# Optimization experiments

Hardware: AMD Instinct MI355X
Metric: run time of the kernel (lower is better)

## Reference

```python
import jax, jax.numpy as jnp
import numpy as np
from jax.scipy.special import logsumexp

D, V, B, N = 256, 10000, 16, 22
CF, CR, CA = 400, 120, 48   # num_func_cats, num_res_cats, num_arg_cats
NEG = -1e9


def setup_inputs() -> dict:
    key = jax.random.key(0)
    ks = jax.random.split(key, 12)
    s = 0.1
    return {
        "fake_emb": jnp.eye(CR, dtype=jnp.float32),  # nn.Parameter(torch.eye(num_res_cats))
        "nt_emb": jax.random.normal(ks[0], (CF, D), jnp.float32),
        "rule_W": jax.random.normal(ks[1], (2 * CA, CR), jnp.float32) * s,
        "rule_b": jnp.zeros((2 * CA,), jnp.float32),
        "root_w": jax.random.normal(ks[2], (CF,), jnp.float32) * s,  # root_mlp weight (input dim 1)
        "root_b": jnp.zeros((CF,), jnp.float32),
        "root_mask": jnp.zeros((CF,), jnp.float32),  # can_be_root mask (0 = allowed)
        "split_W1": jax.random.normal(ks[3], (D, D), jnp.float32) * s,
        "split_b1": jnp.zeros((D,), jnp.float32),
        "res_W": jax.random.normal(ks[4], (2, 2, D, D), jnp.float32) * s,  # 2 ResidualLayers x 2 Linears
        "res_b": jnp.zeros((2, 2, D), jnp.float32),
        "split_Wo": jax.random.normal(ks[5], (D, 2), jnp.float32) * s,
        "split_bo": jnp.zeros((2,), jnp.float32),
        "emit_W": jax.random.normal(ks[6], (D, V), jnp.float32) * s,  # word emission head
        "emit_b": jnp.zeros((V,), jnp.float32),
        "words": jax.random.randint(ks[7], (B, N), 0, V),
        "lfunc_ixs": jax.random.randint(ks[8], (CR, CA), 0, CF),
        "rfunc_ixs": jax.random.randint(ks[9], (CR, CA), 0, CF),
    }


def reference(fake_emb, nt_emb, rule_W, rule_b, root_w, root_b, root_mask,
              split_W1, split_b1, res_W, res_b, split_Wo, split_bo,
              emit_W, emit_b, words, lfunc_ixs, rfunc_ixs):
    # ---- grammar scores (set_grammar branch) ----
    # root_mlp(eye(1)).squeeze() == root_w + root_b
    root_scores = jax.nn.log_softmax(root_mask + root_w + root_b)          # [CF]
    rule_scores = jax.nn.log_softmax(fake_emb @ rule_W.T + rule_b, axis=1)  # [CR, 2*CA]

    # split_mlp: Linear -> ResidualLayer x2 -> Linear(D,2)
    h = nt_emb @ split_W1 + split_b1
    for i in range(2):  # fixed small layer loop
        t = jax.nn.relu(h @ res_W[i, 0] + res_b[i, 0])
        h = jax.nn.relu(t @ res_W[i, 1] + res_b[i, 1]) + h
    split_scores = jax.nn.log_softmax(h @ split_Wo + split_bo, axis=1)      # [CF, 2]

    gL = rule_scores[:, :CA] + split_scores[:CR, 0:1]  # full_G_larg [CR, CA]
    gR = rule_scores[:, CA:] + split_scores[:CR, 0:1]  # full_G_rarg [CR, CA]

    # ---- emission model: log p(word | category) gathered per token ----
    word_lp = jax.nn.log_softmax(nt_emb @ emit_W + emit_b, axis=-1)  # [CF, V]
    emit = word_lp[:, words]                                         # [CF, B, N]
    term = (split_scores[:, 1][:, None, None] + emit).transpose(2, 1, 0)  # [N, B, CF]

    # ---- CKY inside pass: beta[i, j, b, cat] over spans ----
    beta = jnp.full((N, N, B, CF), NEG, jnp.float32)
    d = jnp.arange(N)
    beta = beta.at[d, d].set(term)

    for w in range(2, N + 1):  # recurrence over span widths (static)
        S = N - w + 1
        st = np.arange(S)[:, None]          # span starts [S,1]
        kk = np.arange(1, w)[None, :]       # split points [1,w-1]
        left = beta[st, st + kk - 1]                                   # [S,w-1,B,CF]
        right = beta[st + kk, np.broadcast_to(st + w - 1, (S, w - 1))]  # [S,w-1,B,CF]
        # res -> arg(left) + rfunc(right)
        sL = gL + left[..., :CA][..., None, :] + right[..., rfunc_ixs]  # [S,w-1,B,CR,CA]
        # res -> lfunc(left) + arg(right)
        sR = gR + left[..., lfunc_ixs] + right[..., :CA][..., None, :]
        new = jnp.logaddexp(logsumexp(sL, axis=(1, 4)),
                            logsumexp(sR, axis=(1, 4)))                 # [S,B,CR]
        full = jnp.full((S, B, CF), NEG, jnp.float32).at[..., :CR].set(new)
        beta = beta.at[st[:, 0], st[:, 0] + w - 1].set(full)

    ll = logsumexp(root_scores + beta[0, N - 1], axis=-1)  # [B]
    return -ll  # logprob_list * -1
```

## Files before the change

kernel.cpp:

```cpp
#include <hip/hip_runtime.h>
#include <math.h>

#define D 256
#define V 10000
#define BB 16
#define NN 22
#define CF 400
#define CR 120
#define CA 48
#define CRP 121
#define PADF 20

__global__ void k_root(const float* __restrict__ root_w, const float* __restrict__ root_b,
                       const float* __restrict__ root_mask, float* __restrict__ root_scores) {
  __shared__ float red[512];
  int t = threadIdx.x;
  float x = (t < CF) ? (root_mask[t] + root_w[t] + root_b[t]) : -INFINITY;
  red[t] = x; __syncthreads();
  for (int off = 256; off; off >>= 1) { if (t < off) red[t] = fmaxf(red[t], red[t + off]); __syncthreads(); }
  float m = red[0]; __syncthreads();
  red[t] = (t < CF) ? __expf(x - m) : 0.f; __syncthreads();
  for (int off = 256; off; off >>= 1) { if (t < off) red[t] += red[t + off]; __syncthreads(); }
  float z = m + __logf(red[0]);
  if (t < CF) root_scores[t] = x - z;
}

__global__ __launch_bounds__(512) void k_mlp(const float* __restrict__ nt_emb, const float* __restrict__ W1,
                      const float* __restrict__ b1, const float* __restrict__ resW,
                      const float* __restrict__ resb, const float* __restrict__ Wo,
                      const float* __restrict__ bo, float* __restrict__ split_scores) {
  __shared__ float xs[2][D], hs[2][D], ts[2][D], prt[2][2][D];
  __shared__ float redg[2][4][2];
  int t = threadIdx.x; int c = t & 255; int h = t >> 8;
  int f0 = blockIdx.x * 2;
  xs[h][c] = nt_emb[(size_t)(f0 + h) * D + c];
  __syncthreads();
  int d0 = h * 128;
  float a0 = 0.f, a1 = 0.f;
#pragma unroll 8
  for (int dd = 0; dd < 128; dd++) {
    float wv = W1[(size_t)(d0 + dd) * D + c];
    a0 += xs[0][d0 + dd] * wv; a1 += xs[1][d0 + dd] * wv;
  }
  prt[0][h][c] = a0; prt[1][h][c] = a1;
  __syncthreads();
  if (h == 0) {
    float bv = b1[c];
    hs[0][c] = prt[0][0][c] + prt[0][1][c] + bv;
    hs[1][c] = prt[1][0][c] + prt[1][1][c] + bv;
  }
  __syncthreads();
  for (int il = 0; il < 2; il++) {
    const float* W = resW + (size_t)(il * 2) * D * D;
    a0 = 0.f; a1 = 0.f;
#pragma unroll 8
    for (int dd = 0; dd < 128; dd++) {
      float wv = W[(size_t)(d0 + dd) * D + c];
      a0 += hs[0][d0 + dd] * wv; a1 += hs[1][d0 + dd] * wv;
    }
    prt[0][h][c] = a0; prt[1][h][c] = a1;
    __syncthreads();
    if (h == 0) {
      float bv = resb[(il * 2) * D + c];
      ts[0][c] = fmaxf(prt[0][0][c] + prt[0][1][c] + bv, 0.f);
      ts[1][c] = fmaxf(prt[1][0][c] + prt[1][1][c] + bv, 0.f);
    }
    __syncthreads();
    const float* W2 = resW + (size_t)(il * 2 + 1) * D * D;
    a0 = 0.f; a1 = 0.f;
#pragma unroll 8
    for (int dd = 0; dd < 128; dd++) {
      float wv = W2[(size_t)(d0 + dd) * D + c];
      a0 += ts[0][d0 + dd] * wv; a1 += ts[1][d0 + dd] * wv;
    }
    prt[0][h][c] = a0; prt[1][h][c] = a1;
    __syncthreads();
    if (h == 0) {
      float bv = resb[(il * 2 + 1) * D + c];
      hs[0][c] = fmaxf(prt[0][0][c] + prt[0][1][c] + bv, 0.f) + hs[0][c];
      hs[1][c] = fmaxf(prt[1][0][c] + prt[1][1][c] + bv, 0.f) + hs[1][c];
    }
    __syncthreads();
  }
  float y0 = hs[h][c] * Wo[c * 2 + 0], y1 = hs[h][c] * Wo[c * 2 + 1];
  for (int off = 32; off; off >>= 1) { y0 += __shfl_down(y0, off, 64); y1 += __shfl_down(y1, off, 64); }
  int wq = (t >> 6) & 3;
  if ((t & 63) == 0) { redg[h][wq][0] = y0; redg[h][wq][1] = y1; }
  __syncthreads();
  if (c == 0) {
    float s0 = redg[h][0][0] + redg[h][1][0] + redg[h][2][0] + redg[h][3][0] + bo[0];
    float s1 = redg[h][0][1] + redg[h][1][1] + redg[h][2][1] + redg[h][3][1] + bo[1];
    float m = fmaxf(s0, s1);
    float z = m + __logf(__expf(s0 - m) + __expf(s1 - m));
    split_scores[(f0 + h) * 2 + 0] = s0 - z;
    split_scores[(f0 + h) * 2 + 1] = s1 - z;
  }
}

__global__ void k_glgr(const float* __restrict__ rule_W, const float* __restrict__ rule_b,
                       const float* __restrict__ split_scores,
                       const int* __restrict__ lf, const int* __restrict__ rf,
                       float4* __restrict__ rules) {
  __shared__ float red[128];
  __shared__ float shv[96];
  int r = blockIdx.x;
  int t = threadIdx.x;
  float x = (t < 96) ? (rule_W[t * CR + r] + rule_b[t]) : -INFINITY;
  red[t] = x; __syncthreads();
  for (int off = 64; off; off >>= 1) { if (t < off) red[t] = fmaxf(red[t], red[t + off]); __syncthreads(); }
  float m = red[0]; __syncthreads();
  red[t] = (t < 96) ? __expf(x - m) : 0.f; __syncthreads();
  for (int off = 64; off; off >>= 1) { if (t < off) red[t] += red[t + off]; __syncthreads(); }
  float z = m + __logf(red[0]);
  float s0 = split_scores[r * 2 + 0];
  if (t < 96) shv[t] = __expf((x - z) + s0);
  __syncthreads();
  if (t < CA) {
    float4 pk;
    pk.x = shv[t];
    pk.y = shv[CA + t];
    pk.z = __int_as_float(rf[r * CA + t]);
    pk.w = __int_as_float(lf[r * CA + t]);
    rules[r * CA + t] = pk;
  }
}

#define RT 8
__global__ __launch_bounds__(128) void k_emit_partial(const float* __restrict__ nt_emb,
                               const float* __restrict__ emit_W,
                               const float* __restrict__ emit_b, float* __restrict__ partial) {
  __shared__ float xs[RT][D];
  __shared__ float ldsw[RT][2];
  int t = threadIdx.x;
  int f0 = blockIdx.x * RT;
  int v0 = blockIdx.y * 512 + t * 4;
  for (int idx = t; idx < RT * D; idx += 128) {
    int ri = idx >> 8, d = idx & 255;
    xs[ri][d] = nt_emb[(size_t)(f0 + ri) * D + d];
  }
  __syncthreads();
  float psum[RT];
  for (int ri = 0; ri < RT; ri++) psum[ri] = 0.f;
  if (v0 < V) {
    float acc[RT][4];
#pragma unroll
    for (int ri = 0; ri < RT; ri++)
      for (int j = 0; j < 4; j++) acc[ri][j] = 0.f;
    for (int d4 = 0; d4 < D / 4; d4++) {
      float4 w0 = *(const float4*)(emit_W + (size_t)(4 * d4 + 0) * V + v0);
      float4 w1 = *(const float4*)(emit_W + (size_t)(4 * d4 + 1) * V + v0);
      float4 w2 = *(const float4*)(emit_W + (size_t)(4 * d4 + 2) * V + v0);
      float4 w3 = *(const float4*)(emit_W + (size_t)(4 * d4 + 3) * V + v0);
#pragma unroll
      for (int ri = 0; ri < RT; ri++) {
        float4 xv = *(const float4*)(&xs[ri][4 * d4]);
        acc[ri][0] += xv.x * w0.x + xv.y * w1.x + xv.z * w2.x + xv.w * w3.x;
        acc[ri][1] += xv.x * w0.y + xv.y * w1.y + xv.z * w2.y + xv.w * w3.y;
        acc[ri][2] += xv.x * w0.z + xv.y * w1.z + xv.z * w2.z + xv.w * w3.z;
        acc[ri][3] += xv.x * w0.w + xv.y * w1.w + xv.z * w2.w + xv.w * w3.w;
      }
    }
    float4 eb = *(const float4*)(emit_b + v0);
#pragma unroll
    for (int ri = 0; ri < RT; ri++)
      psum[ri] = __expf(acc[ri][0] + eb.x) + __expf(acc[ri][1] + eb.y) +
                 __expf(acc[ri][2] + eb.z) + __expf(acc[ri][3] + eb.w);
  }
  int lane = t & 63, wid = t >> 6;
  for (int ri = 0; ri < RT; ri++) {
    float v = psum[ri];
    for (int off = 32; off; off >>= 1) v += __shfl_down(v, off, 64);
    if (lane == 0) ldsw[ri][wid] = v;
  }
  __syncthreads();
  if (t < RT) partial[(f0 + t) * 32 + blockIdx.y] = ldsw[t][0] + ldsw[t][1];
}

__global__ void k_logz(const float* __restrict__ partial, float* __restrict__ logZ) {
  int t = blockIdx.x * blockDim.x + threadIdx.x;
  if (t < CF) {
    float s = 0.f;
    for (int ct = 0; ct < 20; ct++) s += partial[t * 32 + ct];
    logZ[t] = __logf(s);
  }
}

__global__ __launch_bounds__(512) void k_term(const float* __restrict__ nt_emb,
                       const float* __restrict__ emit_W,
                       const float* __restrict__ emit_b, const int* __restrict__ words,
                       const float* __restrict__ split_scores, const float* __restrict__ logZ,
                       float* __restrict__ ET, float* __restrict__ bmax) {
  __shared__ float vals[CF];
  __shared__ float redw[8];
  __shared__ float mfin;
  int blk = blockIdx.x;
  int b = blk / NN, n = blk % NN;
  int t = threadIdx.x;
  int lane = t & 63, wid = t >> 6;
  int wd = words[b * NN + n];
  float wc0 = emit_W[(size_t)(4 * lane + 0) * V + wd];
  float wc1 = emit_W[(size_t)(4 * lane + 1) * V + wd];
  float wc2 = emit_W[(size_t)(4 * lane + 2) * V + wd];
  float wc3 = emit_W[(size_t)(4 * lane + 3) * V + wd];
  float eb = emit_b[wd];
  float vmax = -INFINITY;
  int fbase = wid * 50;
  for (int k = 0; k < 50; k += 2) {
    int f0 = fbase + k, f1 = f0 + 1;
    float4 xa = *(const float4*)(nt_emb + (size_t)f0 * D + 4 * lane);
    float4 xb = *(const float4*)(nt_emb + (size_t)f1 * D + 4 * lane);
    float va = xa.x * wc0 + xa.y * wc1 + xa.z * wc2 + xa.w * wc3;
    float vb = xb.x * wc0 + xb.y * wc1 + xb.z * wc2 + xb.w * wc3;
    for (int off = 32; off; off >>= 1) {
      va += __shfl_down(va, off, 64);
      vb += __shfl_down(vb, off, 64);
    }
    if (lane == 0) {
      float fa = split_scores[f0 * 2 + 1] + (va + eb) - logZ[f0];
      float fb = split_scores[f1 * 2 + 1] + (vb + eb) - logZ[f1];
      vals[f0] = fa; vals[f1] = fb;
      vmax = fmaxf(vmax, fmaxf(fa, fb));
    }
  }
  if (lane == 0) redw[wid] = vmax;
  __syncthreads();
  if (t == 0) {
    float m = redw[0];
    for (int i2 = 1; i2 < 8; i2++) m = fmaxf(m, redw[i2]);
    mfin = m;
    bmax[(n * NN + n) * BB + b] = m;
  }
  __syncthreads();
  float m = mfin;
  for (int f = t; f < CF; f += 512) ET[((size_t)n * CF + f) * BB + b] = __expf(vals[f] - m);
}

__global__ __launch_bounds__(512) void k_cky_part(const float4* __restrict__ rules,
                      const float* __restrict__ ET, const float* __restrict__ EB,
                      const float* __restrict__ bmax, float* __restrict__ partial,
                      int w, int rsplit) {
  __shared__ float SL[CF * PADF];
  __shared__ float SR[CF * PADF];
  __shared__ float sMbuf[21 * BB];
  __shared__ float cks[BB];
  __shared__ float4 sred[512];
  int t = threadIdx.x;
  int blk = blockIdx.x;
  int rb = blk % rsplit; int rem = blk / rsplit;
  int wm1 = w - 1;
  int k = rem % wm1; int s = rem / wm1;
  int i = s, j = s + w - 1;
  bool ld = (k == 0), rd = (k == wm1 - 1);
  if (t < BB * wm1) {
    int k2 = t >> 4, b2 = t & 15;
    sMbuf[t] = bmax[(i * NN + (i + k2)) * BB + b2] + bmax[((i + k2 + 1) * NN + j) * BB + b2];
  }
  __syncthreads();
  if (t < BB) {
    float M = sMbuf[t];
    for (int k2 = 1; k2 < wm1; k2++) M = fmaxf(M, sMbuf[k2 * BB + t]);
    cks[t] = __expf(sMbuf[k * BB + t] - M);
  }
  const float* srcL = ld ? (ET + (size_t)i * CF * BB) : (EB + (size_t)(i * NN + (i + k)) * CRP * BB);
  const float* srcR = rd ? (ET + (size_t)j * CF * BB) : (EB + (size_t)((i + k + 1) * NN + j) * CRP * BB);
  int rowsL = ld ? CF : CRP, rowsR = rd ? CF : CRP;
  for (int idx = t; idx < rowsL * 4; idx += 512) {
    int f = idx >> 2, q = idx & 3;
    *(float4*)&SL[f * PADF + q * 4] = *(const float4*)&srcL[f * BB + q * 4];
  }
  for (int idx = t; idx < rowsR * 4; idx += 512) {
    int f = idx >> 2, q = idx & 3;
    *(float4*)&SR[f * PADF + q * 4] = *(const float4*)&srcR[f * BB + q * 4];
  }
  __syncthreads();
  int nr = CR / rsplit;
  int asplit = 128 / nr;
  int bq = t & 3, rr = t >> 2;
  float4 acc = {0.f, 0.f, 0.f, 0.f};
  bool act = (rr < nr * asplit);
  int rloc = rr % nr, asub = rr / nr;
  int r = rb * nr + rloc;
  if (act) {
    int na = CA / asplit;
    const float4* rp = rules + (size_t)r * CA + asub * na;
    int boff = bq * 4;
    int aB = asub * na;
#pragma unroll 4
    for (int a0 = 0; a0 < na; a0++) {
      float4 rule = rp[a0];
      int a = aB + a0;
      int fL = __float_as_int(rule.z);
      int fR = __float_as_int(rule.w);
      int fLc = rd ? fL : min(fL, 120);
      int fRc = ld ? fR : min(fR, 120);
      float4 La = *(const float4*)&SL[a * PADF + boff];
      float4 Ra = *(const float4*)&SR[a * PADF + boff];
      float4 Rg = *(const float4*)&SR[fLc * PADF + boff];
      float4 Lg = *(const float4*)&SL[fRc * PADF + boff];
      acc.x += rule.x * (La.x * Rg.x) + rule.y * (Lg.x * Ra.x);
      acc.y += rule.x * (La.y * Rg.y) + rule.y * (Lg.y * Ra.y);
      acc.z += rule.x * (La.z * Rg.z) + rule.y * (Lg.z * Ra.z);
      acc.w += rule.x * (La.w * Rg.w) + rule.y * (Lg.w * Ra.w);
    }
  }
  if (asplit > 1) {
    sred[t] = acc;
    __syncthreads();
    if (act && asub == 0) {
      for (int s2 = 1; s2 < asplit; s2++) {
        float4 o = sred[t + s2 * nr * 4];
        acc.x += o.x; acc.y += o.y; acc.z += o.z; acc.w += o.w;
      }
    }
  }
  if (act && asub == 0) {
    float4 c4 = *(const float4*)&cks[bq * 4];
    acc.x *= c4.x; acc.y *= c4.y; acc.z *= c4.z; acc.w *= c4.w;
    *(float4*)&partial[(((size_t)s * 21 + k) * CR + r) * BB + bq * 4] = acc;
  }
}

__global__ __launch_bounds__(512) void k_cky_comb(const float* __restrict__ partial,
                      float* __restrict__ EB, float* __restrict__ bmax, int w) {
  __shared__ float sums[CR * BB];
  __shared__ float sMbuf[21 * BB];
  __shared__ float msum[BB];
  __shared__ float Mb[BB];
  int t = threadIdx.x;
  int s = blockIdx.x;
  int i = s, j = s + w - 1;
  int wm1 = w - 1;
  if (t < BB * wm1) {
    int k2 = t >> 4, b2 = t & 15;
    sMbuf[t] = bmax[(i * NN + (i + k2)) * BB + b2] + bmax[((i + k2 + 1) * NN + j) * BB + b2];
  }
  __syncthreads();
  if (t < BB) {
    float M = sMbuf[t];
    for (int k2 = 1; k2 < wm1; k2++) M = fmaxf(M, sMbuf[k2 * BB + t]);
    Mb[t] = M;
  }
  int bq = t & 3, rr = t >> 2;
  float4 sum = {0.f, 0.f, 0.f, 0.f};
  if (rr < CR) {
    for (int k2 = 0; k2 < wm1; k2++) {
      float4 p = *(const float4*)&partial[(((size_t)s * 21 + k2) * CR + rr) * BB + bq * 4];
      sum.x += p.x; sum.y += p.y; sum.z += p.z; sum.w += p.w;
    }
    *(float4*)&sums[rr * BB + bq * 4] = sum;
  }
  __syncthreads();
  if (t < BB) {
    float m = 0.f;
    for (int r2 = 0; r2 < CR; r2++) m = fmaxf(m, sums[r2 * BB + t]);
    m = fmaxf(m, 1e-35f);
    msum[t] = m;
    bmax[(i * NN + j) * BB + t] = Mb[t] + __logf(m);
  }
  __syncthreads();
  if (rr < CR) {
    float4 m4 = *(const float4*)&msum[bq * 4];
    sum.x /= m4.x; sum.y /= m4.y; sum.z /= m4.z; sum.w /= m4.w;
    *(float4*)&EB[(((size_t)i * NN + j) * CRP + rr) * BB + bq * 4] = sum;
  }
  if (t < BB) EB[(((size_t)i * NN + j) * CRP + 120) * BB + t] = 0.f;
}

__global__ void k_final(const float* __restrict__ root_scores, const float* __restrict__ EB,
                        const float* __restrict__ bmax, float* __restrict__ out) {
  __shared__ float red[128];
  int b = blockIdx.x;
  int t = threadIdx.x;
  float x = (t < CR) ? __expf(root_scores[t]) * EB[(((size_t)0 * NN + (NN - 1)) * CRP + t) * BB + b] : 0.f;
  red[t] = x; __syncthreads();
  for (int off = 64; off; off >>= 1) { if (t < off) red[t] += red[t + off]; __syncthreads(); }
  if (t == 0) out[b] = -(bmax[(0 * NN + (NN - 1)) * BB + b] + __logf(red[0]));
}

extern "C" void kernel_launch(void* const* d_in, const int* in_sizes, int n_in,
                              void* d_out, int out_size, void* d_ws, size_t ws_size,
                              hipStream_t stream) {
  const float* nt_emb   = (const float*)d_in[1];
  const float* rule_W   = (const float*)d_in[2];
  const float* rule_b   = (const float*)d_in[3];
  const float* root_w   = (const float*)d_in[4];
  const float* root_b   = (const float*)d_in[5];
  const float* root_mask= (const float*)d_in[6];
  const float* split_W1 = (const float*)d_in[7];
  const float* split_b1 = (const float*)d_in[8];
  const float* res_W    = (const float*)d_in[9];
  const float* res_b    = (const float*)d_in[10];
  const float* split_Wo = (const float*)d_in[11];
  const float* split_bo = (const float*)d_in[12];
  const float* emit_W   = (const float*)d_in[13];
  const float* emit_b   = (const float*)d_in[14];
  const int*   words    = (const int*)d_in[15];
  const int*   lfunc    = (const int*)d_in[16];
  const int*   rfunc    = (const int*)d_in[17];

  float* ws = (float*)d_ws;
  float* ET           = ws;
  float* EB           = ET + NN * CF * BB;
  float* bmaxbuf      = EB + NN * NN * CRP * BB;
  float* partialK     = bmaxbuf + NN * NN * BB;
  float* rules        = partialK + 21 * 21 * CR * BB;
  float* root_scores  = rules + CR * CA * 4;
  float* split_scores = root_scores + CF;
  float* logZ         = split_scores + 2 * CF;
  float* partialE     = logZ + CF;

  hipLaunchKernelGGL(k_root, dim3(1), dim3(512), 0, stream, root_w, root_b, root_mask, root_scores);
  hipLaunchKernelGGL(k_mlp, dim3(CF / 2), dim3(512), 0, stream, nt_emb, split_W1, split_b1,
                     res_W, res_b, split_Wo, split_bo, split_scores);
  hipLaunchKernelGGL(k_glgr, dim3(CR), dim3(128), 0, stream, rule_W, rule_b, split_scores,
                     lfunc, rfunc, (float4*)rules);
  hipLaunchKernelGGL(k_emit_partial, dim3(CF / RT, 20), dim3(128), 0, stream, nt_emb, emit_W, emit_b, partialE);
  hipLaunchKernelGGL(k_logz, dim3(2), dim3(256), 0, stream, partialE, logZ);
  hipLaunchKernelGGL(k_term, dim3(BB * NN), dim3(512), 0, stream, nt_emb, emit_W, emit_b,
                     words, split_scores, logZ, ET, bmaxbuf);
  for (int w = 2; w <= NN; w++) {
    int S = NN - w + 1;
    int units = S * (w - 1);
    int rsplit = (units >= 224) ? 1 : ((units >= 112) ? 2 : 4);
    hipLaunchKernelGGL(k_cky_part, dim3(units * rsplit), dim3(512), 0, stream,
                       (const float4*)rules, ET, EB, bmaxbuf, partialK, w, rsplit);
    hipLaunchKernelGGL(k_cky_comb, dim3(S), dim3(512), 0, stream, partialK, EB, bmaxbuf, w);
  }
  hipLaunchKernelGGL(k_final, dim3(BB), dim3(128), 0, stream, root_scores, EB, bmaxbuf, (float*)d_out);
}
```

Before: 375.1 us.

## Fuse CKY part/combine via atomic last-block reduction and merge small kernels

Fuses the per-width CKY partial and combine kernels into one launch: every block writes its partial, bumps an atomic counter per span, and the last block to arrive performs the combine and resets the counter. Root log-softmax moves into k_final and the logZ reduction into an extra k_glgr block, and the emission GEMM grid is remapped so that blocks are spread across XCDs. The aim is to cut about 24 kernel launches and their inter-kernel gaps on a latency-bound recurrence. In exchange it adds threadfence and atomic overhead and serialises the combine inside one block per span, and it relies on the counter buffer starting at zero, which the glgr block resets.

```diff
diff --git a/kernel.cpp b/kernel.cpp
--- a/kernel.cpp
+++ b/kernel.cpp
@@ -11,20 +11,6 @@
 #define CRP 121
 #define PADF 20
 
-__global__ void k_root(const float* __restrict__ root_w, const float* __restrict__ root_b,
-                       const float* __restrict__ root_mask, float* __restrict__ root_scores) {
-  __shared__ float red[512];
-  int t = threadIdx.x;
-  float x = (t < CF) ? (root_mask[t] + root_w[t] + root_b[t]) : -INFINITY;
-  red[t] = x; __syncthreads();
-  for (int off = 256; off; off >>= 1) { if (t < off) red[t] = fmaxf(red[t], red[t + off]); __syncthreads(); }
-  float m = red[0]; __syncthreads();
-  red[t] = (t < CF) ? __expf(x - m) : 0.f; __syncthreads();
-  for (int off = 256; off; off >>= 1) { if (t < off) red[t] += red[t + off]; __syncthreads(); }
-  float z = m + __logf(red[0]);
-  if (t < CF) root_scores[t] = x - z;
-}
-
 __global__ __launch_bounds__(512) void k_mlp(const float* __restrict__ nt_emb, const float* __restrict__ W1,
                       const float* __restrict__ b1, const float* __restrict__ resW,
                       const float* __restrict__ resb, const float* __restrict__ Wo,
@@ -97,43 +83,22 @@
   }
 }
 
-__global__ void k_glgr(const float* __restrict__ rule_W, const float* __restrict__ rule_b,
-                       const float* __restrict__ split_scores,
-                       const int* __restrict__ lf, const int* __restrict__ rf,
-                       float4* __restrict__ rules) {
-  __shared__ float red[128];
-  __shared__ float shv[96];
-  int r = blockIdx.x;
-  int t = threadIdx.x;
-  float x = (t < 96) ? (rule_W[t * CR + r] + rule_b[t]) : -INFINITY;
-  red[t] = x; __syncthreads();
-  for (int off = 64; off; off >>= 1) { if (t < off) red[t] = fmaxf(red[t], red[t + off]); __syncthreads(); }
-  float m = red[0]; __syncthreads();
-  red[t] = (t < 96) ? __expf(x - m) : 0.f; __syncthreads();
-  for (int off = 64; off; off >>= 1) { if (t < off) red[t] += red[t + off]; __syncthreads(); }
-  float z = m + __logf(red[0]);
-  float s0 = split_scores[r * 2 + 0];
-  if (t < 96) shv[t] = __expf((x - z) + s0);
-  __syncthreads();
-  if (t < CA) {
-    float4 pk;
-    pk.x = shv[t];
-    pk.y = shv[CA + t];
-    pk.z = __int_as_float(rf[r * CA + t]);
-    pk.w = __int_as_float(lf[r * CA + t]);
-    rules[r * CA + t] = pk;
-  }
-}
-
 #define RT 8
 __global__ __launch_bounds__(128) void k_emit_partial(const float* __restrict__ nt_emb,
                                const float* __restrict__ emit_W,
                                const float* __restrict__ emit_b, float* __restrict__ partial) {
   __shared__ float xs[RT][D];
   __shared__ float ldsw[RT][2];
+  int bid = blockIdx.x;
+  int xcd = bid & 7;
+  int rest = bid >> 3;
+  int xt = rest % 50;
+  int yh = rest / 50;
+  int y = yh * 8 + xcd;
+  if (y >= 20) return;
   int t = threadIdx.x;
-  int f0 = blockIdx.x * RT;
-  int v0 = blockIdx.y * 512 + t * 4;
+  int f0 = xt * RT;
+  int v0 = y * 512 + t * 4;
   for (int idx = t; idx < RT * D; idx += 128) {
     int ri = idx >> 8, d = idx & 255;
     xs[ri][d] = nt_emb[(size_t)(f0 + ri) * D + d];
@@ -141,11 +106,12 @@
   __syncthreads();
   float psum[RT];
   for (int ri = 0; ri < RT; ri++) psum[ri] = 0.f;
-  if (v0 < V) {
+  {
     float acc[RT][4];
 #pragma unroll
     for (int ri = 0; ri < RT; ri++)
       for (int j = 0; j < 4; j++) acc[ri][j] = 0.f;
+#pragma unroll 2
     for (int d4 = 0; d4 < D / 4; d4++) {
       float4 w0 = *(const float4*)(emit_W + (size_t)(4 * d4 + 0) * V + v0);
       float4 w1 = *(const float4*)(emit_W + (size_t)(4 * d4 + 1) * V + v0);
@@ -173,15 +139,44 @@
     if (lane == 0) ldsw[ri][wid] = v;
   }
   __syncthreads();
-  if (t < RT) partial[(f0 + t) * 32 + blockIdx.y] = ldsw[t][0] + ldsw[t][1];
-}
-
-__global__ void k_logz(const float* __restrict__ partial, float* __restrict__ logZ) {
-  int t = blockIdx.x * blockDim.x + threadIdx.x;
-  if (t < CF) {
-    float s = 0.f;
-    for (int ct = 0; ct < 20; ct++) s += partial[t * 32 + ct];
-    logZ[t] = __logf(s);
+  if (t < RT) partial[(f0 + t) * 32 + y] = ldsw[t][0] + ldsw[t][1];
+}
+
+__global__ void k_glgr(const float* __restrict__ rule_W, const float* __restrict__ rule_b,
+                       const float* __restrict__ split_scores,
+                       const int* __restrict__ lf, const int* __restrict__ rf,
+                       const float* __restrict__ partialE, float* __restrict__ logZ,
+                       int* __restrict__ cnt, float4* __restrict__ rules) {
+  __shared__ float red[128];
+  __shared__ float shv[96];
+  int r = blockIdx.x;
+  int t = threadIdx.x;
+  if (r == CR) {
+    for (int f = t; f < CF; f += 128) {
+      float s = 0.f;
+      for (int ct = 0; ct < 20; ct++) s += partialE[f * 32 + ct];
+      logZ[f] = __logf(s);
+    }
+    if (t < 32) cnt[t] = 0;
+    return;
+  }
+  float x = (t < 96) ? (rule_W[t * CR + r] + rule_b[t]) : -INFINITY;
+  red[t] = x; __syncthreads();
+  for (int off = 64; off; off >>= 1) { if (t < off) red[t] = fmaxf(red[t], red[t + off]); __syncthreads(); }
+  float m = red[0]; __syncthreads();
+  red[t] = (t < 96) ? __expf(x - m) : 0.f; __syncthreads();
+  for (int off = 64; off; off >>= 1) { if (t < off) red[t] += red[t + off]; __syncthreads(); }
+  float z = m + __logf(red[0]);
+  float s0 = split_scores[r * 2 + 0];
+  if (t < 96) shv[t] = __expf((x - z) + s0);
+  __syncthreads();
+  if (t < CA) {
+    float4 pk;
+    pk.x = shv[t];
+    pk.y = shv[CA + t];
+    pk.z = __int_as_float(rf[r * CA + t]);
+    pk.w = __int_as_float(lf[r * CA + t]);
+    rules[r * CA + t] = pk;
   }
 }
 
@@ -235,15 +230,20 @@
   for (int f = t; f < CF; f += 512) ET[((size_t)n * CF + f) * BB + b] = __expf(vals[f] - m);
 }
 
-__global__ __launch_bounds__(512) void k_cky_part(const float4* __restrict__ rules,
-                      const float* __restrict__ ET, const float* __restrict__ EB,
-                      const float* __restrict__ bmax, float* __restrict__ partial,
-                      int w, int rsplit) {
-  __shared__ float SL[CF * PADF];
-  __shared__ float SR[CF * PADF];
-  __shared__ float sMbuf[21 * BB];
-  __shared__ float cks[BB];
-  __shared__ float4 sred[512];
+__global__ __launch_bounds__(512) void k_cky_fused(const float4* __restrict__ rules,
+                      const float* __restrict__ ET, float* __restrict__ EB,
+                      float* __restrict__ bmax, float* __restrict__ partial,
+                      int* __restrict__ cnt, int w, int rsplit) {
+  __shared__ float lds[16384];
+  float* SL    = lds;
+  float* SR    = lds + 8000;
+  float* sMbuf = lds + 16000;
+  float* Mb    = lds + 16336;
+  float* msum  = lds + 16352;
+  int*   flagp = (int*)&lds[16368];
+  float4* sred = (float4*)lds;
+  float*  sums = lds;
+
   int t = threadIdx.x;
   int blk = blockIdx.x;
   int rb = blk % rsplit; int rem = blk / rsplit;
@@ -259,7 +259,7 @@
   if (t < BB) {
     float M = sMbuf[t];
     for (int k2 = 1; k2 < wm1; k2++) M = fmaxf(M, sMbuf[k2 * BB + t]);
-    cks[t] = __expf(sMbuf[k * BB + t] - M);
+    Mb[t] = M;
   }
   const float* srcL = ld ? (ET + (size_t)i * CF * BB) : (EB + (size_t)(i * NN + (i + k)) * CRP * BB);
   const float* srcR = rd ? (ET + (size_t)j * CF * BB) : (EB + (size_t)((i + k + 1) * NN + j) * CRP * BB);
@@ -304,6 +304,7 @@
     }
   }
   if (asplit > 1) {
+    __syncthreads();
     sred[t] = acc;
     __syncthreads();
     if (act && asub == 0) {
@@ -314,33 +315,21 @@
     }
   }
   if (act && asub == 0) {
-    float4 c4 = *(const float4*)&cks[bq * 4];
-    acc.x *= c4.x; acc.y *= c4.y; acc.z *= c4.z; acc.w *= c4.w;
-    *(float4*)&partial[(((size_t)s * 21 + k) * CR + r) * BB + bq * 4] = acc;
-  }
-}
-
-__global__ __launch_bounds__(512) void k_cky_comb(const float* __restrict__ partial,
-                      float* __restrict__ EB, float* __restrict__ bmax, int w) {
-  __shared__ float sums[CR * BB];
-  __shared__ float sMbuf[21 * BB];
-  __shared__ float msum[BB];
-  __shared__ float Mb[BB];
-  int t = threadIdx.x;
-  int s = blockIdx.x;
-  int i = s, j = s + w - 1;
-  int wm1 = w - 1;
-  if (t < BB * wm1) {
-    int k2 = t >> 4, b2 = t & 15;
-    sMbuf[t] = bmax[(i * NN + (i + k2)) * BB + b2] + bmax[((i + k2 + 1) * NN + j) * BB + b2];
-  }
-  __syncthreads();
-  if (t < BB) {
-    float M = sMbuf[t];
-    for (int k2 = 1; k2 < wm1; k2++) M = fmaxf(M, sMbuf[k2 * BB + t]);
-    Mb[t] = M;
-  }
-  int bq = t & 3, rr = t >> 2;
+    int b0 = bq * 4;
+    acc.x *= __expf(sMbuf[k * BB + b0 + 0] - Mb[b0 + 0]);
+    acc.y *= __expf(sMbuf[k * BB + b0 + 1] - Mb[b0 + 1]);
+    acc.z *= __expf(sMbuf[k * BB + b0 + 2] - Mb[b0 + 2]);
+    acc.w *= __expf(sMbuf[k * BB + b0 + 3] - Mb[b0 + 3]);
+    *(float4*)&partial[(((size_t)s * 21 + k) * CR + r) * BB + b0] = acc;
+  }
+  __threadfence();
+  __syncthreads();
+  if (t == 0) *flagp = atomicAdd(&cnt[s], 1);
+  __syncthreads();
+  int kparts = wm1 * rsplit;
+  if (*flagp != kparts - 1) return;
+  __threadfence();
+  __syncthreads();
   float4 sum = {0.f, 0.f, 0.f, 0.f};
   if (rr < CR) {
     for (int k2 = 0; k2 < wm1; k2++) {
@@ -364,14 +353,33 @@
     *(float4*)&EB[(((size_t)i * NN + j) * CRP + rr) * BB + bq * 4] = sum;
   }
   if (t < BB) EB[(((size_t)i * NN + j) * CRP + 120) * BB + t] = 0.f;
-}
-
-__global__ void k_final(const float* __restrict__ root_scores, const float* __restrict__ EB,
-                        const float* __restrict__ bmax, float* __restrict__ out) {
+  if (t == 0) cnt[s] = 0;
+}
+
+__global__ __launch_bounds__(128) void k_final(const float* __restrict__ root_w,
+                        const float* __restrict__ root_b, const float* __restrict__ root_mask,
+                        const float* __restrict__ EB, const float* __restrict__ bmax,
+                        float* __restrict__ out) {
   __shared__ float red[128];
   int b = blockIdx.x;
   int t = threadIdx.x;
-  float x = (t < CR) ? __expf(root_scores[t]) * EB[(((size_t)0 * NN + (NN - 1)) * CRP + t) * BB + b] : 0.f;
+  float xv[4];
+  float lm = -INFINITY;
+  for (int kq = 0; kq < 4; kq++) {
+    int f = t + kq * 128;
+    xv[kq] = (f < CF) ? (root_mask[f] + root_w[f] + root_b[f]) : -INFINITY;
+    lm = fmaxf(lm, xv[kq]);
+  }
+  red[t] = lm; __syncthreads();
+  for (int off = 64; off; off >>= 1) { if (t < off) red[t] = fmaxf(red[t], red[t + off]); __syncthreads(); }
+  float M = red[0]; __syncthreads();
+  float le = 0.f;
+  for (int kq = 0; kq < 4; kq++) le += (t + kq * 128 < CF) ? __expf(xv[kq] - M) : 0.f;
+  red[t] = le; __syncthreads();
+  for (int off = 64; off; off >>= 1) { if (t < off) red[t] += red[t + off]; __syncthreads(); }
+  float z = M + __logf(red[0]);
+  __syncthreads();
+  float x = (t < CR) ? __expf(xv[0] - z) * EB[(((size_t)0 * NN + (NN - 1)) * CRP + t) * BB + b] : 0.f;
   red[t] = x; __syncthreads();
   for (int off = 64; off; off >>= 1) { if (t < off) red[t] += red[t + off]; __syncthreads(); }
   if (t == 0) out[b] = -(bmax[(0 * NN + (NN - 1)) * BB + b] + __logf(red[0]));
@@ -404,27 +412,25 @@
   float* bmaxbuf      = EB + NN * NN * CRP * BB;
   float* partialK     = bmaxbuf + NN * NN * BB;
   float* rules        = partialK + 21 * 21 * CR * BB;
-  float* root_scores  = rules + CR * CA * 4;
-  float* split_scores = root_scores + CF;
+  float* split_scores = rules + CR * CA * 4;
   float* logZ         = split_scores + 2 * CF;
   float* partialE     = logZ + CF;
-
-  hipLaunchKernelGGL(k_root, dim3(1), dim3(512), 0, stream, root_w, root_b, root_mask, root_scores);
+  int*   cnt          = (int*)(partialE + CF * 32);
+
   hipLaunchKernelGGL(k_mlp, dim3(CF / 2), dim3(512), 0, stream, nt_emb, split_W1, split_b1,
                      res_W, res_b, split_Wo, split_bo, split_scores);
-  hipLaunchKernelGGL(k_glgr, dim3(CR), dim3(128), 0, stream, rule_W, rule_b, split_scores,
-                     lfunc, rfunc, (float4*)rules);
-  hipLaunchKernelGGL(k_emit_partial, dim3(CF / RT, 20), dim3(128), 0, stream, nt_emb, emit_W, emit_b, partialE);
-  hipLaunchKernelGGL(k_logz, dim3(2), dim3(256), 0, stream, partialE, logZ);
+  hipLaunchKernelGGL(k_emit_partial, dim3(1200), dim3(128), 0, stream, nt_emb, emit_W, emit_b, partialE);
+  hipLaunchKernelGGL(k_glgr, dim3(CR + 1), dim3(128), 0, stream, rule_W, rule_b, split_scores,
+                     lfunc, rfunc, partialE, logZ, cnt, (float4*)rules);
   hipLaunchKernelGGL(k_term, dim3(BB * NN), dim3(512), 0, stream, nt_emb, emit_W, emit_b,
                      words, split_scores, logZ, ET, bmaxbuf);
   for (int w = 2; w <= NN; w++) {
     int S = NN - w + 1;
     int units = S * (w - 1);
     int rsplit = (units >= 224) ? 1 : ((units >= 112) ? 2 : 4);
-    hipLaunchKernelGGL(k_cky_part, dim3(units * rsplit), dim3(512), 0, stream,
-                       (const float4*)rules, ET, EB, bmaxbuf, partialK, w, rsplit);
-    hipLaunchKernelGGL(k_cky_comb, dim3(S), dim3(512), 0, stream, partialK, EB, bmaxbuf, w);
-  }
-  hipLaunchKernelGGL(k_final, dim3(BB), dim3(128), 0, stream, root_scores, EB, bmaxbuf, (float*)d_out);
-}
+    hipLaunchKernelGGL(k_cky_fused, dim3(units * rsplit), dim3(512), 0, stream,
+                       (const float4*)rules, ET, EB, bmaxbuf, partialK, cnt, w, rsplit);
+  }
+  hipLaunchKernelGGL(k_final, dim3(BB), dim3(128), 0, stream, root_w, root_b, root_mask,
+                     EB, bmaxbuf, (float*)d_out);
+}
```

New measurement: 1.226 ms. 227% more time.
